# Optimization experiments

Measured on AMD Instinct MI355X. Metric: run time of the kernel, lower is better.

Reference implementation:

```python
import jax, jax.numpy as jnp
import numpy as np

M, K, L, C = 8, 4, 2, 128
C_v = C // M


def _bilinear(img, gx, gy):
    # img: [N, C_v, h, w]; gx, gy: [N, K, H, W] normalized grid coords in [-1, 1]
    # torch F.grid_sample(mode='bilinear', padding_mode='zeros', align_corners=False)
    N, Cc, h, w = img.shape
    ix = ((gx + 1.0) * w - 1.0) * 0.5
    iy = ((gy + 1.0) * h - 1.0) * 0.5
    x0 = jnp.floor(ix)
    y0 = jnp.floor(iy)
    wx1 = ix - x0
    wy1 = iy - y0
    wx0 = 1.0 - wx1
    wy0 = 1.0 - wy1

    def gather(xs, ys):
        valid = ((xs >= 0) & (xs < w) & (ys >= 0) & (ys < h)).astype(img.dtype)
        xc = jnp.clip(xs, 0, w - 1).astype(jnp.int32)
        yc = jnp.clip(ys, 0, h - 1).astype(jnp.int32)
        v = jax.vmap(lambda im, y, x: im[:, y, x])(img, yc, xc)  # [N, C_v, K, H, W]
        return v * valid[:, None]

    out = (gather(x0, y0) * (wx0 * wy0)[:, None]
           + gather(x0 + 1.0, y0) * (wx1 * wy0)[:, None]
           + gather(x0, y0 + 1.0) * (wx0 * wy1)[:, None]
           + gather(x0 + 1.0, y0 + 1.0) * (wx1 * wy1)[:, None])
    return out  # [N, C_v, K, H, W]


def _forward(z_q, x0, x1, p_q, Wq, bq, Wd, bd, Wa, ba, Wp, bp, Wm, bm):
    B, H, W, _ = z_q.shape
    zq = z_q @ Wq + bq
    # sampling offsets and attention weights
    deltas = (zq @ Wd + bd).reshape(B, H, W, M, L, K, 2)
    A = jax.nn.softmax((zq @ Wa + ba).reshape(B, H, W, M, L * K), axis=-1)
    # deltas -> [B*M, L, K, H, W, 2]; A -> [B*M, H*W, L*K]
    d = jnp.transpose(deltas, (0, 3, 4, 5, 1, 2, 6)).reshape(B * M, L, K, H, W, 2)
    An = jnp.transpose(A, (0, 3, 1, 2, 4)).reshape(B * M, H * W, L * K)
    pq = jax.lax.stop_gradient(p_q)  # phi() detaches p_q in the original

    samples = []
    for l, xl in enumerate([x0, x1]):
        h, w = xl.shape[1], xl.shape[2]
        phi = pq * jnp.array([w - 1.0, h - 1.0], dtype=z_q.dtype)  # phi(w,h,p_q)
        # NOTE: torch .repeat(M,1,1,1) tiles batch as m*B+b (replicated faithfully)
        phi = jnp.tile(phi, (M, 1, 1, 1))  # [M*B, H, W, 2]
        Wx = (xl @ Wp + bp).reshape(B, h, w, M, C_v)
        Wx = jnp.transpose(Wx, (0, 3, 4, 1, 2)).reshape(B * M, C_v, h, w)
        coords = phi[:, None] + d[:, l]  # [B*M, K, H, W, 2]
        gx = 2.0 * coords[..., 0] / max(w - 1, 1) - 1.0
        gy = 2.0 * coords[..., 1] / max(h - 1, 1) - 1.0
        s = _bilinear(Wx, gx, gy)  # [B*M, C_v, K, H, W]
        # original stacks per-k samples at dim=3 -> [B*M, C_v, H, K, W]
        samples.append(jnp.transpose(s, (0, 1, 3, 2, 4)))
    S = jnp.stack(samples, axis=1)  # [B*M, L, C_v, H, K, W]
    # faithful to original permute(0,4,5,3,1,2).view(B*M, H*W, C_v, L*K)
    S = jnp.transpose(S, (0, 4, 5, 3, 1, 2)).reshape(B * M, H * W, C_v, L * K)
    out = jnp.einsum('nlds,nls->nld', S, An)  # [B*M, H*W, C_v]
    out = out.reshape(B, M, H, W, C_v)
    out = jnp.transpose(out, (0, 2, 3, 1, 4)).reshape(B, H, W, M * C_v)
    return out @ Wm + bm


def setup_inputs() -> dict:
    key = jax.random.key(0)
    ks = jax.random.split(key, 14)
    B, H, W = 2, 128, 128
    s = 0.02
    return {
        'z_q': jax.random.normal(ks[0], (B, H, W, C), jnp.float32),
        'x0': jax.random.normal(ks[1], (B, 64, 64, C), jnp.float32),
        'x1': jax.random.normal(ks[2], (B, 128, 128, C), jnp.float32),
        'p_q': jax.random.uniform(ks[3], (B, H, W, 2), jnp.float32),
        'Wq': jax.random.normal(ks[4], (C, C), jnp.float32) * s,
        'bq': jnp.zeros((C,), jnp.float32),
        'Wd': jax.random.normal(ks[5], (C, 2 * M * K * L), jnp.float32) * s,
        'bd': jax.random.normal(ks[6], (2 * M * K * L,), jnp.float32),
        'Wa': jax.random.normal(ks[7], (C, M * K * L), jnp.float32) * s,
        'ba': jnp.full((M * K * L,), 1.0 / (L * K), jnp.float32),
        'Wp': jax.random.normal(ks[8], (C, C), jnp.float32) * s,
        'bp': jnp.zeros((C,), jnp.float32),
        'Wm': jax.random.normal(ks[9], (C, C), jnp.float32) * s,
        'bm': jnp.zeros((C,), jnp.float32),
    }


def reference(z_q, x0, x1, p_q, Wq, bq, Wd, bd, Wa, ba, Wp, bp, Wm, bm):
    return _forward(z_q, x0, x1, p_q, Wq, bq, Wd, bd, Wa, ba, Wp, bp, Wm, bm)
```

## Files before the change

kernel.cpp:

```cpp
#include <hip/hip_runtime.h>
#include <hip/hip_bf16.h>

constexpr int CB = 2;
constexpr int CH = 128;
constexpr int CW = 128;
constexpr int CM = 8;

typedef __bf16 bf16x8 __attribute__((ext_vector_type(8)));
typedef float  f32x4  __attribute__((ext_vector_type(4)));
typedef unsigned short us8 __attribute__((ext_vector_type(8)));
typedef unsigned short us4 __attribute__((ext_vector_type(4)));

__device__ __forceinline__ unsigned short f2bf(float f) {
  __hip_bfloat16 h = __float2bfloat16(f);
  return *reinterpret_cast<unsigned short*>(&h);
}
__device__ __forceinline__ float bf2f(unsigned short u) {
  union { unsigned int i; float f; } v;
  v.i = ((unsigned int)u) << 16;
  return v.f;
}

__global__ __launch_bounds__(256) void prep_all_kernel(
    const float* __restrict__ Wq, const float* __restrict__ bq,
    const float* __restrict__ Wd, const float* __restrict__ bd,
    const float* __restrict__ Wa, const float* __restrict__ ba,
    const float* __restrict__ Wp, const float* __restrict__ Wm,
    unsigned short* __restrict__ WtDA, unsigned short* __restrict__ WtP,
    unsigned short* __restrict__ WtM, float* __restrict__ bda)
{
  const int blk = blockIdx.x, t = threadIdx.x;
  if (blk < 384) {
    const int gtid = blk * 256 + t;
    const int idx = gtid >> 2;
    const int kc  = gtid & 3;
    const int j = idx >> 7, k = idx & 127;
    const int i0 = kc * 32;
    float s = 0.f;
    if (j < 128) {
#pragma unroll
      for (int i = 0; i < 32; ++i)
        s = fmaf(Wq[k * 128 + i0 + i], Wd[(i0 + i) * 128 + j], s);
    } else {
#pragma unroll
      for (int i = 0; i < 32; ++i)
        s = fmaf(Wq[k * 128 + i0 + i], Wa[(i0 + i) * 64 + (j - 128)], s);
    }
    s += __shfl_xor(s, 1);
    s += __shfl_xor(s, 2);
    if (kc == 0) WtDA[j * 128 + k] = f2bf(s);
  } else if (blk < 448) {
    int idx = (blk - 384) * 256 + t;
    {
      const int k = idx >> 7, j = idx & 127;
      WtP[j * 128 + k] = f2bf(Wp[idx]);
    }
    {
      const int k = idx >> 7, j = idx & 127;
      WtM[j * 128 + k] = f2bf(Wm[idx]);
    }
  } else {
    if (t < 192) {
      const int j = t;
      float s = (j < 128) ? bd[j] : ba[j - 128];
      if (j < 128) {
#pragma unroll 8
        for (int i = 0; i < 128; ++i) s = fmaf(bq[i], Wd[i * 128 + j], s);
      } else {
#pragma unroll 8
        for (int i = 0; i < 128; ++i) s = fmaf(bq[i], Wa[i * 64 + (j - 128)], s);
      }
      bda[j] = s;
    }
  }
}

__device__ __forceinline__ void stage_B(const unsigned short* __restrict__ src,
                                        unsigned short* __restrict__ lds,
                                        int n_us8)
{
  for (int v = threadIdx.x; v < n_us8; v += 256) {
    const us8 d = *(const us8*)(src + v * 8);
    const int col = v >> 4;
    const int slot = (v & 15) ^ (col & 7);
    *(us8*)(lds + col * 128 + slot * 8) = d;
  }
}
__device__ __forceinline__ bf16x8 lds_frag(const unsigned short* __restrict__ lds,
                                           int rc, int ko)
{
  const int slot = (ko >> 3) ^ (rc & 7);
  return *(const bf16x8*)(lds + rc * 128 + slot * 8);
}

__global__ __launch_bounds__(256) void pre_gemm_kernel(
    const float* __restrict__ z_q, const float* __restrict__ x0,
    const float* __restrict__ x1,
    const unsigned short* __restrict__ WtDA, const float* __restrict__ bda,
    const unsigned short* __restrict__ WtP,  const float* __restrict__ bp,
    float* __restrict__ dl2, float* __restrict__ Alog,
    unsigned short* __restrict__ Wx, int nZv)
{
  __shared__ __align__(16) unsigned short smem[24576];

  const int t  = threadIdx.x;
  const int w  = t >> 6;
  const int l  = t & 63;
  const int lr = l & 15;
  const int kg = l >> 4;
  const int blk = blockIdx.x;

  if (blk < nZv) {
    unsigned short* Bsh = smem;
    unsigned short* Ahi = smem + 12288;
    const int r0 = (blk >> 1) * 64;
    const int cg = blk & 1;

    stage_B(WtDA + cg * 96 * 128, Bsh, 1536);
    {
      const float4* Ag = (const float4*)(z_q + (size_t)r0 * 128);
#pragma unroll
      for (int i = 0; i < 8; ++i) {
        const int v = t + i * 256;
        const float4 f = Ag[v];
        const int flat = v * 4;
        const int row = flat >> 7;
        const int ko  = flat & 127;
        us4 h;
        h[0] = f2bf(f.x); h[1] = f2bf(f.y); h[2] = f2bf(f.z); h[3] = f2bf(f.w);
        *(us4*)(Ahi + row * 128 + (((ko >> 3) ^ (row & 7)) << 3) + (ko & 7)) = h;
      }
    }
    __syncthreads();

    f32x4 acc[6];
#pragma unroll
    for (int jt = 0; jt < 6; ++jt) acc[jt] = (f32x4){0.f, 0.f, 0.f, 0.f};

    const int lrow = w * 16 + lr;
#pragma unroll
    for (int k0 = 0; k0 < 128; k0 += 32) {
      const int ko = k0 + kg * 8;
      const bf16x8 ah = lds_frag(Ahi, lrow, ko);
#pragma unroll
      for (int jt = 0; jt < 6; ++jt) {
        const bf16x8 bh = lds_frag(Bsh, jt * 16 + lr, ko);
        acc[jt] = __builtin_amdgcn_mfma_f32_16x16x32_bf16(ah, bh, acc[jt], 0, 0, 0);
      }
    }

    const int scol = ((lr >> 1) & 3) * 32 + ((lr >> 3) & 1) * 2 + (lr & 1);
#pragma unroll
    for (int jt = 0; jt < 6; ++jt) {
      const int jtg = cg * 6 + jt;
      if (jtg < 8) {
        const float bv = bda[jtg * 16 + lr];
#pragma unroll
        for (int ri = 0; ri < 4; ++ri) {
          const int row = r0 + w * 16 + kg * 4 + ri;
          dl2[(size_t)row * 128 + jtg * 4 + scol] = acc[jt][ri] + bv;
        }
      } else {
        const int col = (jtg - 8) * 16 + lr;
        const float bv = bda[128 + col];
#pragma unroll
        for (int ri = 0; ri < 4; ++ri) {
          const int row = r0 + w * 16 + kg * 4 + ri;
          Alog[(size_t)row * 64 + col] = acc[jt][ri] + bv;
        }
      }
    }
  } else {
    unsigned short* Bsh = smem;
    unsigned short* Ahi = smem + 8192;
    unsigned short* Alo = smem + 16384;
    const int i = blk - nZv;
    const int r0 = (i >> 1) * 64;
    const int cg = i & 1;
    const float* A = (r0 < 8192) ? (x0 + (size_t)r0 * 128)
                                 : (x1 + (size_t)(r0 - 8192) * 128);

    stage_B(WtP + cg * 64 * 128, Bsh, 1024);
    {
      const float4* Ag = (const float4*)A;
#pragma unroll
      for (int ii = 0; ii < 8; ++ii) {
        const int v = t + ii * 256;
        const float4 f = Ag[v];
        const int flat = v * 4;
        const int row = flat >> 7;
        const int ko  = flat & 127;
        const float ff[4] = {f.x, f.y, f.z, f.w};
        us4 h, lo;
#pragma unroll
        for (int u = 0; u < 4; ++u) {
          h[u]  = f2bf(ff[u]);
          lo[u] = f2bf(ff[u] - bf2f(h[u]));
        }
        const int off = row * 128 + (((ko >> 3) ^ (row & 7)) << 3) + (ko & 7);
        *(us4*)(Ahi + off) = h;
        *(us4*)(Alo + off) = lo;
      }
    }
    __syncthreads();

    f32x4 acc[4];
#pragma unroll
    for (int jt = 0; jt < 4; ++jt) acc[jt] = (f32x4){0.f, 0.f, 0.f, 0.f};

    const int lrow = w * 16 + lr;
#pragma unroll
    for (int k0 = 0; k0 < 128; k0 += 32) {
      const int ko = k0 + kg * 8;
      const bf16x8 ah = lds_frag(Ahi, lrow, ko);
      const bf16x8 al = lds_frag(Alo, lrow, ko);
#pragma unroll
      for (int jt = 0; jt < 4; ++jt) {
        const bf16x8 bh = lds_frag(Bsh, jt * 16 + lr, ko);
        acc[jt] = __builtin_amdgcn_mfma_f32_16x16x32_bf16(ah, bh, acc[jt], 0, 0, 0);
        acc[jt] = __builtin_amdgcn_mfma_f32_16x16x32_bf16(al, bh, acc[jt], 0, 0, 0);
      }
    }

#pragma unroll
    for (int jt = 0; jt < 4; ++jt) {
      const int col = cg * 64 + jt * 16 + lr;
      const float bv = bp[col];
#pragma unroll
      for (int ri = 0; ri < 4; ++ri) {
        const int row = r0 + w * 16 + kg * 4 + ri;
        Wx[(size_t)row * 128 + col] = f2bf(acc[jt][ri] + bv);
      }
    }
  }
}

__global__ __launch_bounds__(256) void final_gemm_kernel(
    const unsigned short* __restrict__ Pbf,
    const unsigned short* __restrict__ WtM,
    const float* __restrict__ bm, float* __restrict__ out)
{
  __shared__ __align__(16) unsigned short smem[16384];
  unsigned short* Bsh = smem;
  unsigned short* Ash = smem + 8192;

  const int t  = threadIdx.x;
  const int w  = t >> 6;
  const int l  = t & 63;
  const int lr = l & 15;
  const int kg = l >> 4;
  const int r0 = (blockIdx.x >> 1) * 64;
  const int cg = blockIdx.x & 1;

  stage_B(WtM + cg * 64 * 128, Bsh, 1024);
  stage_B(Pbf + (size_t)r0 * 128, Ash, 1024);
  __syncthreads();

  f32x4 acc[4];
#pragma unroll
  for (int jt = 0; jt < 4; ++jt) acc[jt] = (f32x4){0.f, 0.f, 0.f, 0.f};

  const int lrow = w * 16 + lr;
#pragma unroll
  for (int k0 = 0; k0 < 128; k0 += 32) {
    const int ko = k0 + kg * 8;
    const bf16x8 av = lds_frag(Ash, lrow, ko);
#pragma unroll
    for (int jt = 0; jt < 4; ++jt) {
      const bf16x8 bh = lds_frag(Bsh, jt * 16 + lr, ko);
      acc[jt] = __builtin_amdgcn_mfma_f32_16x16x32_bf16(av, bh, acc[jt], 0, 0, 0);
    }
  }

#pragma unroll
  for (int jt = 0; jt < 4; ++jt) {
    const int col = cg * 64 + jt * 16 + lr;
    const float bv = bm[col];
#pragma unroll
    for (int ri = 0; ri < 4; ++ri) {
      const int row = r0 + w * 16 + kg * 4 + ri;
      out[(size_t)row * 128 + col] = acc[jt][ri] + bv;
    }
  }
}

__global__ __launch_bounds__(128) void sample_attn_kernel(
    const float* __restrict__ Alog,
    const float* __restrict__ dl2,
    const float* __restrict__ p_q,
    const unsigned short* __restrict__ Wx,
    unsigned short* __restrict__ Pbf)
{
  const int bid = blockIdx.x;
  const int q = (bid & 7) * 4096 + (bid >> 3);
  const int w = q & (CW - 1);
  const int h = (q >> 7) & (CH - 1);
  const int b = q >> 14;
  const int t = threadIdx.x;
  const int m = t >> 4;
  const int c = t & 15;

  const int kk   = h >> 5;
  const int xp   = (w >> 5) + ((h & 31) << 2);
  const int yp   = (c >> 2) + ((w & 31) << 2);
  const int lp   = (c >> 1) & 1;
  const int half = c & 1;

  const size_t qp = ((size_t)b * CH + yp) * CW + xp;
  const float2 dxy = *(const float2*)(dl2 + qp * 128 + kk * 32 + m * 4 + lp * 2);

  const int pb = (b * CM + m) % CB;
  const float2 pq2 = *(const float2*)(p_q + ((((size_t)pb * CH + yp) * CW + xp) * 2));

  const float* al = Alog + (size_t)q * 64 + m * 8;
  const float4 al0 = ((const float4*)al)[0];
  const float4 al1 = ((const float4*)al)[1];

  const int wl = lp ? 128 : 64;
  const int hl = wl;
  const int imgbase = lp ? (8192 + b * 16384) : (b * 4096);

  const float cx = pq2.x * (float)(wl - 1) + dxy.x;
  const float cy = pq2.y * (float)(hl - 1) + dxy.y;
  const float gx = 2.f * cx / (float)(wl - 1) - 1.f;
  const float gy = 2.f * cy / (float)(hl - 1) - 1.f;
  const float ix = ((gx + 1.f) * (float)wl - 1.f) * 0.5f;
  const float iy = ((gy + 1.f) * (float)hl - 1.f) * 0.5f;
  const float x0f = floorf(ix), y0f = floorf(iy);
  const float fx1 = ix - x0f, fy1 = iy - y0f;
  const float fx0 = 1.f - fx1, fy0 = 1.f - fy1;
  const int xi = (int)x0f, yi = (int)y0f;

  const float vx0 = ((unsigned)xi < (unsigned)wl) ? 1.f : 0.f;
  const float vx1 = ((unsigned)(xi + 1) < (unsigned)wl) ? 1.f : 0.f;
  const float vy0 = ((unsigned)yi < (unsigned)hl) ? 1.f : 0.f;
  const float vy1 = ((unsigned)(yi + 1) < (unsigned)hl) ? 1.f : 0.f;
  const int xc0 = min(max(xi, 0), wl - 1);
  const int xc1 = min(max(xi + 1, 0), wl - 1);
  const int yc0 = min(max(yi, 0), hl - 1);
  const int yc1 = min(max(yi + 1, 0), hl - 1);

  const unsigned short* base = Wx + (size_t)imgbase * 128 + (m * 16 + half * 8);
  const unsigned short* p00 = base + (size_t)(yc0 * wl + xc0) * 128;
  const unsigned short* p01 = base + (size_t)(yc0 * wl + xc1) * 128;
  const unsigned short* p10 = base + (size_t)(yc1 * wl + xc0) * 128;
  const unsigned short* p11 = base + (size_t)(yc1 * wl + xc1) * 128;

  const us8 g00 = *(const us8*)p00;
  const us8 g01 = *(const us8*)p01;
  const us8 g10 = *(const us8*)p10;
  const us8 g11 = *(const us8*)p11;

  float lg[8] = {al0.x, al0.y, al0.z, al0.w, al1.x, al1.y, al1.z, al1.w};
  float mx = -3.0e38f;
#pragma unroll
  for (int s = 0; s < 8; ++s) mx = fmaxf(mx, lg[s]);
  float se = 0.f;
#pragma unroll
  for (int s = 0; s < 8; ++s) { lg[s] = __expf(lg[s] - mx); se += lg[s]; }
  const float inv = 1.f / se;

  const float w00 = fy0 * fx0 * vy0 * vx0;
  const float w01 = fy0 * fx1 * vy0 * vx1;
  const float w10 = fy1 * fx0 * vy1 * vx0;
  const float w11 = fy1 * fx1 * vy1 * vx1;

  float o = 0.f;
#pragma unroll
  for (int s = 0; s < 8; ++s) {
    float v = w00 * bf2f(g00[s]);
    v = fmaf(w01, bf2f(g01[s]), v);
    v = fmaf(w10, bf2f(g10[s]), v);
    v = fmaf(w11, bf2f(g11[s]), v);
    o = fmaf(lg[s] * inv, v, o);
  }
  Pbf[(size_t)q * 128 + t] = f2bf(o);
}

extern "C" void kernel_launch(void* const* d_in, const int* in_sizes, int n_in,
                              void* d_out, int out_size, void* d_ws, size_t ws_size,
                              hipStream_t stream)
{
  const float* z_q = (const float*)d_in[0];
  const float* x0  = (const float*)d_in[1];
  const float* x1  = (const float*)d_in[2];
  const float* p_q = (const float*)d_in[3];
  const float* Wq  = (const float*)d_in[4];
  const float* bq  = (const float*)d_in[5];
  const float* Wd  = (const float*)d_in[6];
  const float* bd  = (const float*)d_in[7];
  const float* Wa  = (const float*)d_in[8];
  const float* ba  = (const float*)d_in[9];
  const float* Wp  = (const float*)d_in[10];
  const float* bp  = (const float*)d_in[11];
  const float* Wm  = (const float*)d_in[12];
  const float* bm  = (const float*)d_in[13];

  float* ws = (float*)d_ws;
  const int NQ = CB * CH * CW;

  unsigned short* Wts  = (unsigned short*)ws;
  unsigned short* WtDA = Wts;
  unsigned short* WtP  = Wts + 24576;
  unsigned short* WtM  = Wts + 40960;
  float* bda = ws + 28672;

  float* dl2  = ws + 28864;
  float* Alog = dl2 + 4194304;
  unsigned short* Wx  = (unsigned short*)(Alog + 2097152);
  unsigned short* Pbf = Wx + 5242880;

  prep_all_kernel<<<449, 256, 0, stream>>>(Wq, bq, Wd, bd, Wa, ba, Wp, Wm,
                                           WtDA, WtP, WtM, bda);

  const int nZv = 1024;
  pre_gemm_kernel<<<nZv + 1280, 256, 0, stream>>>(z_q, x0, x1, WtDA, bda,
                                                  WtP, bp, dl2, Alog, Wx, nZv);

  sample_attn_kernel<<<NQ, 128, 0, stream>>>(Alog, dl2, p_q, Wx, Pbf);

  final_gemm_kernel<<<NQ / 32, 256, 0, stream>>>(Pbf, WtM, bm, (float*)d_out);
}
```

Measured before the change: 182.8 us.

## Process four queries per block with each thread handling two channels

The sampling kernel now runs 256-thread blocks that each cover four queries. Each thread computes one set of bilinear coordinates and reads 16 contiguous bf16 channels, where before it read 8. This halves the redundant coordinate, softmax and index arithmetic per output channel and writes packed 32-bit outputs. The cost is fewer threads overall and more registers per thread, with the same total gather traffic.

```diff
diff --git a/kernel.cpp b/kernel.cpp
--- a/kernel.cpp
+++ b/kernel.cpp
@@ -284,7 +284,7 @@
   }
 }
 
-__global__ __launch_bounds__(128) void sample_attn_kernel(
+__global__ __launch_bounds__(256) void sample_attn_kernel(
     const float* __restrict__ Alog,
     const float* __restrict__ dl2,
     const float* __restrict__ p_q,
@@ -292,24 +292,27 @@
     unsigned short* __restrict__ Pbf)
 {
   const int bid = blockIdx.x;
-  const int q = (bid & 7) * 4096 + (bid >> 3);
+  const int t  = threadIdx.x;
+  const int qi = t >> 6;
+  const int l  = t & 63;
+  const int m  = l >> 3;
+  const int c2 = l & 7;
+  const int ypo = c2 >> 1;
+  const int lp  = c2 & 1;
+
+  const int q = (bid & 7) * 4096 + (bid >> 3) * 4 + qi;
   const int w = q & (CW - 1);
   const int h = (q >> 7) & (CH - 1);
   const int b = q >> 14;
-  const int t = threadIdx.x;
-  const int m = t >> 4;
-  const int c = t & 15;
-
-  const int kk   = h >> 5;
-  const int xp   = (w >> 5) + ((h & 31) << 2);
-  const int yp   = (c >> 2) + ((w & 31) << 2);
-  const int lp   = (c >> 1) & 1;
-  const int half = c & 1;
+
+  const int kk = h >> 5;
+  const int xp = (w >> 5) + ((h & 31) << 2);
+  const int yp = ypo + ((w & 31) << 2);
 
   const size_t qp = ((size_t)b * CH + yp) * CW + xp;
   const float2 dxy = *(const float2*)(dl2 + qp * 128 + kk * 32 + m * 4 + lp * 2);
 
-  const int pb = (b * CM + m) % CB;
+  const int pb = m & 1;
   const float2 pq2 = *(const float2*)(p_q + ((((size_t)pb * CH + yp) * CW + xp) * 2));
 
   const float* al = Alog + (size_t)q * 64 + m * 8;
@@ -320,10 +323,11 @@
   const int hl = wl;
   const int imgbase = lp ? (8192 + b * 16384) : (b * 4096);
 
-  const float cx = pq2.x * (float)(wl - 1) + dxy.x;
-  const float cy = pq2.y * (float)(hl - 1) + dxy.y;
-  const float gx = 2.f * cx / (float)(wl - 1) - 1.f;
-  const float gy = 2.f * cy / (float)(hl - 1) - 1.f;
+  const float fwl1 = (float)(wl - 1);
+  const float cx = pq2.x * fwl1 + dxy.x;
+  const float cy = pq2.y * fwl1 + dxy.y;
+  const float gx = 2.f * cx / fwl1 - 1.f;
+  const float gy = 2.f * cy / fwl1 - 1.f;
   const float ix = ((gx + 1.f) * (float)wl - 1.f) * 0.5f;
   const float iy = ((gy + 1.f) * (float)hl - 1.f) * 0.5f;
   const float x0f = floorf(ix), y0f = floorf(iy);
@@ -340,16 +344,16 @@
   const int yc0 = min(max(yi, 0), hl - 1);
   const int yc1 = min(max(yi + 1, 0), hl - 1);
 
-  const unsigned short* base = Wx + (size_t)imgbase * 128 + (m * 16 + half * 8);
+  const unsigned short* base = Wx + (size_t)imgbase * 128 + m * 16;
   const unsigned short* p00 = base + (size_t)(yc0 * wl + xc0) * 128;
   const unsigned short* p01 = base + (size_t)(yc0 * wl + xc1) * 128;
   const unsigned short* p10 = base + (size_t)(yc1 * wl + xc0) * 128;
   const unsigned short* p11 = base + (size_t)(yc1 * wl + xc1) * 128;
 
-  const us8 g00 = *(const us8*)p00;
-  const us8 g01 = *(const us8*)p01;
-  const us8 g10 = *(const us8*)p10;
-  const us8 g11 = *(const us8*)p11;
+  const us8 a00 = *(const us8*)p00, b00 = *(const us8*)(p00 + 8);
+  const us8 a01 = *(const us8*)p01, b01 = *(const us8*)(p01 + 8);
+  const us8 a10 = *(const us8*)p10, b10 = *(const us8*)(p10 + 8);
+  const us8 a11 = *(const us8*)p11, b11 = *(const us8*)(p11 + 8);
 
   float lg[8] = {al0.x, al0.y, al0.z, al0.w, al1.x, al1.y, al1.z, al1.w};
   float mx = -3.0e38f;
@@ -365,16 +369,25 @@
   const float w10 = fy1 * fx0 * vy1 * vx0;
   const float w11 = fy1 * fx1 * vy1 * vx1;
 
-  float o = 0.f;
+  float o0 = 0.f, o1 = 0.f;
 #pragma unroll
   for (int s = 0; s < 8; ++s) {
-    float v = w00 * bf2f(g00[s]);
-    v = fmaf(w01, bf2f(g01[s]), v);
-    v = fmaf(w10, bf2f(g10[s]), v);
-    v = fmaf(w11, bf2f(g11[s]), v);
-    o = fmaf(lg[s] * inv, v, o);
-  }
-  Pbf[(size_t)q * 128 + t] = f2bf(o);
+    const float ws = lg[s] * inv;
+    float v0 = w00 * bf2f(a00[s]);
+    v0 = fmaf(w01, bf2f(a01[s]), v0);
+    v0 = fmaf(w10, bf2f(a10[s]), v0);
+    v0 = fmaf(w11, bf2f(a11[s]), v0);
+    o0 = fmaf(ws, v0, o0);
+    float v1 = w00 * bf2f(b00[s]);
+    v1 = fmaf(w01, bf2f(b01[s]), v1);
+    v1 = fmaf(w10, bf2f(b10[s]), v1);
+    v1 = fmaf(w11, bf2f(b11[s]), v1);
+    o1 = fmaf(ws, v1, o1);
+  }
+
+  const unsigned int packed =
+      (unsigned int)f2bf(o0) | ((unsigned int)f2bf(o1) << 16);
+  *(unsigned int*)(Pbf + (size_t)q * 128 + m * 16 + c2 * 2) = packed;
 }
 
 extern "C" void kernel_launch(void* const* d_in, const int* in_sizes, int n_in,
@@ -417,7 +430,7 @@
   pre_gemm_kernel<<<nZv + 1280, 256, 0, stream>>>(z_q, x0, x1, WtDA, bda,
                                                   WtP, bp, dl2, Alog, Wx, nZv);
 
-  sample_attn_kernel<<<NQ, 128, 0, stream>>>(Alog, dl2, p_q, Wx, Pbf);
+  sample_attn_kernel<<<NQ / 4, 256, 0, stream>>>(Alog, dl2, p_q, Wx, Pbf);
 
   final_gemm_kernel<<<NQ / 32, 256, 0, stream>>>(Pbf, WtM, bm, (float*)d_out);
 }
```

Result: slower. 204.9 us (+12.1%).
